# Performance work log

Hardware: AMD Instinct MI355X
Metric: run time of the kernel (lower is better)

## Reference

```python
import jax, jax.numpy as jnp
import numpy as np

NEMBED, EMBED_DIM, HID_DIM, OUT_DIM, NUM_CLASSES = 128, 64, 128, 128, 2
BATCH, TEAM = 2048, 5
N_OPS = 8


def setup_inputs() -> dict:
    key = jax.random.key(0)
    ks = jax.random.split(key, 8)
    w_eq = np.sqrt(2.0 / (EMBED_DIM + HID_DIM + N_OPS))
    return {
        "x": jax.random.randint(ks[0], (BATCH, 2, TEAM), 0, NEMBED, dtype=jnp.int32),
        "embed": jax.random.normal(ks[1], (NEMBED, EMBED_DIM), jnp.float32) * 0.1,
        "coefs1": jax.random.normal(ks[2], (EMBED_DIM, HID_DIM, N_OPS), jnp.float32) * w_eq,
        "bias1": jnp.zeros((HID_DIM,), jnp.float32),
        "wout1": jax.random.normal(ks[3], (HID_DIM, OUT_DIM), jnp.float32) * np.sqrt(1.0 / HID_DIM),
        "bout1": jnp.zeros((OUT_DIM,), jnp.float32),
        "coefs2": jax.random.normal(ks[4], (EMBED_DIM, HID_DIM, N_OPS), jnp.float32) * w_eq,
        "bias2": jnp.zeros((HID_DIM,), jnp.float32),
        "wout2": jax.random.normal(ks[5], (HID_DIM, OUT_DIM), jnp.float32) * np.sqrt(1.0 / HID_DIM),
        "bout2": jnp.zeros((OUT_DIM,), jnp.float32),
        "fcw": jax.random.normal(ks[6], (2 * OUT_DIM, NCLS := NUM_CLASSES and 2 * OUT_DIM and NUM_CLASSES), jnp.float32) * np.sqrt(1.0 / (2 * OUT_DIM)),
        "fcb": jnp.zeros((NUM_CLASSES,), jnp.float32),
    }


def eset_ops_3_to_3(t):
    # t: (N, D, m, m, m). 8 equivariant basis ops: keep-or-(sum&broadcast) each axis.
    # Pooled ops are kept with singleton dims; broadcasting happens after the
    # channel contraction (cheaper, same math as expand-then-contract).
    s1 = t.sum(-3, keepdims=True)
    s2 = t.sum(-2, keepdims=True)
    s3 = t.sum(-1, keepdims=True)
    s12 = t.sum((-3, -2), keepdims=True)
    s13 = t.sum((-3, -1), keepdims=True)
    s23 = t.sum((-2, -1), keepdims=True)
    sall = t.sum((-3, -2, -1), keepdims=True)
    return [t, s1, s2, s3, s12, s13, s23, sall]


def eq3_layer(t, coefs, bias):
    # coefs: (D_in, D_out, 8); output (N, D_out, m, m, m)
    ops = eset_ops_3_to_3(t)
    out = 0.0
    for b, op in enumerate(ops):
        out = out + jnp.einsum('ndijk,ds->nsijk', op, coefs[:, :, b])
    return out + bias[None, :, None, None, None]


def setnet3to3(t, coefs, bias, wout, bout):
    h = jax.nn.relu(eq3_layer(t, coefs, bias))          # (N, H, m, m, m)
    return jnp.einsum('nsijk,so->nijko', h, wout) + bout  # (N, m, m, m, out_dim)


def reference(x, embed, coefs1, bias1, wout1, bout1, coefs2, bias2, wout2, bout2, fcw, fcb):
    e1 = jax.nn.relu(embed[x[:, 0]])  # (N, 5, D)
    e2 = jax.nn.relu(embed[x[:, 1]])
    t1 = jnp.einsum('bid,bjd,bkd->bdijk', e1, e1, e1)  # (N, D, 5, 5, 5)
    t2 = jnp.einsum('bid,bjd,bkd->bdijk', e2, e2, e2)
    o1 = setnet3to3(t1, coefs1, bias1, wout1, bout1)
    o2 = setnet3to3(t2, coefs2, bias2, wout2, bout2)
    t1e = jax.nn.relu(o1.mean(axis=(1, 2, 3)))  # (N, out_dim)
    t2e = jax.nn.relu(o2.mean(axis=(1, 2, 3)))
    z = jnp.concatenate([t1e, t2e], axis=-1)    # dropout_prob=0 / eval mode: no-op
    return z @ fcw + fcb
```

## Files before the change

kernel.cpp:

```cpp
#include <hip/hip_runtime.h>


typedef __attribute__((ext_vector_type(8))) short bf16x8;
typedef __attribute__((ext_vector_type(4))) float f32x4;

#define DEV __device__ __forceinline__

DEV constexpr int pid2(int a, int b) {
  int x = a < b ? a : b;
  int y = a < b ? b : a;
  return x * (9 - x) / 2 + y;
}
DEV constexpr int tid3(int i, int j, int k) {
  int a = i, b = j, c = k, t;
  if (a > b) { t = a; a = b; b = t; }
  if (b > c) { t = b; b = c; c = t; }
  if (a > b) { t = a; a = b; b = t; }
  return a * (a * a - 18 * a + 107) / 6 + (b - a) * (11 - a - b) / 2 + (c - b);
}

DEV ushort f2bf(float f) {
  unsigned u = __builtin_bit_cast(unsigned, f);
  return (ushort)((u + 0x7FFFu + ((u >> 16) & 1u)) >> 16);
}

__global__ __launch_bounds__(256)
void cvt_prep_kernel(const float* __restrict__ c1, const float* __restrict__ c2,
                     const float* __restrict__ w1, const float* __restrict__ w2,
                     ushort* __restrict__ ct, float* __restrict__ wt, int do_wt) {
  const int idx = blockIdx.x * 256 + threadIdx.x;
  if (idx < 2 * 8 * 128 * 64) {
    const int d    = idx & 63;
    const int s    = (idx >> 6) & 127;
    const int b    = (idx >> 13) & 7;
    const int side = idx >> 16;
    const float* src = side ? c2 : c1;
    ct[idx] = f2bf(src[(d * 128 + s) * 8 + b]);
  } else if (do_wt) {
    const int j = idx - 131072;
    if (j < 2 * 128 * 128) {
      const int ss   = j & 127;
      const int o    = (j >> 7) & 127;
      const int side = j >> 14;
      wt[j] = (side ? w2 : w1)[ss * 128 + o];
    }
  }
}


__global__ __launch_bounds__(256, 4)
void dota2_eq3_side(const int* __restrict__ x, const float* __restrict__ embed,
                    const float* __restrict__ bias1, const float* __restrict__ bias2,
                    const float* __restrict__ wout1, const float* __restrict__ wout2,
                    const float* __restrict__ bout1, const float* __restrict__ bout2,
                    const float* __restrict__ fcw,
                    const ushort* __restrict__ ct, const float* __restrict__ wt,
                    float* __restrict__ pbuf)
{
  __shared__ __align__(16) ushort FT[80][72];
  __shared__ __align__(16) float  OUT[64][101];
  __shared__ __align__(16) float  scratch[256];
  __shared__ __align__(16) float  hbar[128];
  __shared__ __align__(16) float  zL[128];

  const int u    = blockIdx.x;
  const int side = u & 1;
  const int tid  = threadIdx.x;
  const int w    = tid >> 6;
  const int l    = tid & 63;
  const int grp  = l >> 4;
  const int lc   = l & 15;

  if (tid < 64) {
    const int d = tid;
    const int* xn = x + u * 5;
    float v[5];
    #pragma unroll
    for (int i = 0; i < 5; ++i) v[i] = fmaxf(embed[xn[i] * 64 + d], 0.f);
    const float S  = v[0] + v[1] + v[2] + v[3] + v[4];
    const float S2 = S * S;
    const float S3 = S2 * S;
    float p2[15];
    {
      int c2 = 0;
      #pragma unroll
      for (int a = 0; a < 5; ++a)
        #pragma unroll
        for (int b = a; b < 5; ++b) { p2[c2] = v[a] * v[b]; ++c2; }
    }
    ushort* colp = &FT[0][d];
    {
      int c3 = 0;
      #pragma unroll
      for (int a = 0; a < 5; ++a)
        #pragma unroll
        for (int b = a; b < 5; ++b)
          #pragma unroll
          for (int c = b; c < 5; ++c) { colp[c3 * 72] = f2bf(p2[pid2(a, b)] * v[c]); ++c3; }
    }
    #pragma unroll
    for (int t = 0; t < 15; ++t) colp[(48 + t) * 72] = f2bf(S * p2[t]);
    #pragma unroll
    for (int i = 0; i < 5; ++i)  colp[(64 + i) * 72] = f2bf(S2 * v[i]);
    colp[69 * 72] = f2bf(S3);
  } else {
    const int idx = tid - 64;
    #pragma unroll
    for (int e0 = 0; e0 < 9; ++e0) {
      const int e = idx + e0 * 192;
      const int r = e / 72;
      const int c = e - r * 72;
      const int row = (r < 13) ? (35 + r) : ((r == 13) ? 63 : (56 + r));
      FT[row][c] = 0;
    }
  }
  __syncthreads();

  const ushort* CTs = ct + side * (8 * 128 * 64);

  auto bfrag = [&](int t0, int kh) -> bf16x8 {
    return *(const bf16x8*)(&FT[t0 + lc][32 * kh + 8 * grp]);
  };
  auto dwrite = [&](const f32x4& acc, int s_local, int colbase, int nvalid) {
    if (lc < nvalid) {
      float* p = &OUT[s_local + 4 * grp][colbase + lc];
      p[0] = acc[0]; p[101] = acc[1]; p[202] = acc[2]; p[303] = acc[3];
    }
  };

  auto do_gemms = [&](int sh) {
    const int sg = 64 * sh + 16 * w;
    const int s_local = 16 * w;
    auto afrag = [&](int b, int kh) -> bf16x8 {
      const ushort* rp = CTs + (b * 128 + sg + lc) * 64;
      return *(const bf16x8*)(rp + 32 * kh + 8 * grp);
    };
    {
      const bf16x8 A0 = afrag(0, 0), A1 = afrag(0, 1);
      #pragma unroll
      for (int nt = 0; nt < 3; ++nt) {
        const bf16x8 B0 = bfrag(nt * 16, 0), B1 = bfrag(nt * 16, 1);
        f32x4 acc = {0.f, 0.f, 0.f, 0.f};
        acc = __builtin_amdgcn_mfma_f32_16x16x32_bf16(A0, B0, acc, 0, 0, 0);
        acc = __builtin_amdgcn_mfma_f32_16x16x32_bf16(A1, B1, acc, 0, 0, 0);
        dwrite(acc, s_local, nt * 16, (nt == 2) ? 3 : 16);
      }
    }
    {
      const bf16x8 B0 = bfrag(48, 0), B1 = bfrag(48, 1);
      #pragma unroll
      for (int b = 1; b <= 3; ++b) {
        const bf16x8 A0 = afrag(b, 0), A1 = afrag(b, 1);
        f32x4 acc = {0.f, 0.f, 0.f, 0.f};
        acc = __builtin_amdgcn_mfma_f32_16x16x32_bf16(A0, B0, acc, 0, 0, 0);
        acc = __builtin_amdgcn_mfma_f32_16x16x32_bf16(A1, B1, acc, 0, 0, 0);
        dwrite(acc, s_local, 35 + (b - 1) * 15, 15);
      }
    }
    {
      const bf16x8 B0 = bfrag(64, 0), B1 = bfrag(64, 1);
      #pragma unroll
      for (int b = 4; b <= 6; ++b) {
        const bf16x8 A0 = afrag(b, 0), A1 = afrag(b, 1);
        f32x4 acc = {0.f, 0.f, 0.f, 0.f};
        acc = __builtin_amdgcn_mfma_f32_16x16x32_bf16(A0, B0, acc, 0, 0, 0);
        acc = __builtin_amdgcn_mfma_f32_16x16x32_bf16(A1, B1, acc, 0, 0, 0);
        dwrite(acc, s_local, 80 + (b - 4) * 5, 5);
      }
      const bf16x8 A0 = afrag(7, 0), A1 = afrag(7, 1);
      f32x4 acc = {0.f, 0.f, 0.f, 0.f};
      acc = __builtin_amdgcn_mfma_f32_16x16x32_bf16(A0, B0, acc, 0, 0, 0);
      acc = __builtin_amdgcn_mfma_f32_16x16x32_bf16(A1, B1, acc, 0, 0, 0);
      if (lc == 5) {
        float* p = &OUT[s_local + 4 * grp][95];
        p[0] = acc[0]; p[101] = acc[1]; p[202] = acc[2]; p[303] = acc[3];
      }
    }
  };

  auto do_asm = [&](int sh) {
    const int ch = tid & 63;
    const int q  = tid >> 6;
    float T[96];
    #pragma unroll
    for (int t = 0; t < 96; ++t) T[t] = OUT[ch][t];
    const float* bi = side ? bias2 : bias1;
    const float base = T[95] + bi[64 * sh + ch];
    float hsum = 0.f;
    auto cell = [&](int c) {
      const int i = c / 25, j = (c / 5) % 5, k = c % 5;
      const float val = base + T[90 + i] + T[85 + j] + T[65 + pid2(i, j)]
                      + T[80 + k] + T[50 + pid2(i, k)] + T[35 + pid2(j, k)]
                      + T[tid3(i, j, k)];
      hsum += fmaxf(val, 0.f);
    };
    if (q == 0) {
      #pragma unroll
      for (int c = 0; c < 31; ++c) cell(c);
    } else if (q == 1) {
      #pragma unroll
      for (int c = 31; c < 62; ++c) cell(c);
    } else if (q == 2) {
      #pragma unroll
      for (int c = 62; c < 93; ++c) cell(c);
    } else {
      #pragma unroll
      for (int c = 93; c < 125; ++c) cell(c);
    }
    scratch[q * 64 + ch] = hsum;
  };

  do_gemms(0);
  __syncthreads();
  do_asm(0);
  __syncthreads();
  if (tid < 64)
    hbar[tid] = (scratch[tid] + scratch[64 + tid] + scratch[128 + tid] + scratch[192 + tid])
                * (1.f / 125.f);
  do_gemms(1);
  __syncthreads();
  do_asm(1);
  __syncthreads();
  if (tid < 64)
    hbar[64 + tid] = (scratch[tid] + scratch[64 + tid] + scratch[128 + tid] + scratch[192 + tid])
                     * (1.f / 125.f);
  __syncthreads();

  {
    const int o = tid & 127, shh = tid >> 7;
    float r;
    if (wt != nullptr) {
      const f32x4* wv = (const f32x4*)(wt + side * 16384 + o * 128 + shh * 64);
      const f32x4* hv = (const f32x4*)(&hbar[shh * 64]);
      float a0 = 0.f, a1 = 0.f, a2 = 0.f, a3 = 0.f;
      #pragma unroll
      for (int qq = 0; qq < 16; ++qq) {
        const f32x4 wq = wv[qq];
        const f32x4 hq = hv[qq];
        a0 = fmaf(hq[0], wq[0], a0);
        a1 = fmaf(hq[1], wq[1], a1);
        a2 = fmaf(hq[2], wq[2], a2);
        a3 = fmaf(hq[3], wq[3], a3);
      }
      r = (a0 + a1) + (a2 + a3);
    } else {
      const float* W = side ? wout2 : wout1;
      float a0 = 0.f, a1 = 0.f;
      #pragma unroll 8
      for (int ss = 64 * shh; ss < 64 * shh + 64; ss += 2) {
        a0 = fmaf(hbar[ss], W[ss * 128 + o], a0);
        a1 = fmaf(hbar[ss + 1], W[(ss + 1) * 128 + o], a1);
      }
      r = a0 + a1;
    }
    scratch[shh * 128 + o] = r;
  }
  __syncthreads();
  if (tid < 128) {
    const float* bo_ = side ? bout2 : bout1;
    zL[tid] = fmaxf(scratch[tid] + scratch[128 + tid] + bo_[tid], 0.f);
  }
  __syncthreads();

  if (tid < 64) {
    const float z0 = zL[tid], z1 = zL[tid + 64];
    const float* fw = fcw + side * 256;
    float p0 = fmaf(z0, fw[2 * tid],     z1 * fw[2 * tid + 128]);
    float p1 = fmaf(z0, fw[2 * tid + 1], z1 * fw[2 * tid + 129]);
    #pragma unroll
    for (int off = 32; off; off >>= 1) {
      p0 += __shfl_down(p0, off);
      p1 += __shfl_down(p1, off);
    }
    if (tid == 0) {
      pbuf[2 * u + 0] = p0;
      pbuf[2 * u + 1] = p1;
    }
  }
}

__global__ __launch_bounds__(256)
void fc_final(const float* __restrict__ pbuf, const float* __restrict__ fcb,
              float* __restrict__ out, int nout) {
  const int t = blockIdx.x * 256 + threadIdx.x;
  if (t < nout) {
    const int n = t >> 1, c = t & 1;
    out[t] = pbuf[4 * n + c] + pbuf[4 * n + 2 + c] + fcb[c];
  }
}

extern "C" void kernel_launch(void* const* d_in, const int* in_sizes, int n_in,
                              void* d_out, int out_size, void* d_ws, size_t ws_size,
                              hipStream_t stream) {
  const int*   x      = (const int*)  d_in[0];
  const float* embed  = (const float*)d_in[1];
  const float* coefs1 = (const float*)d_in[2];
  const float* bias1  = (const float*)d_in[3];
  const float* wout1  = (const float*)d_in[4];
  const float* bout1  = (const float*)d_in[5];
  const float* coefs2 = (const float*)d_in[6];
  const float* bias2  = (const float*)d_in[7];
  const float* wout2  = (const float*)d_in[8];
  const float* bout2  = (const float*)d_in[9];
  const float* fcw    = (const float*)d_in[10];
  const float* fcb    = (const float*)d_in[11];
  float* out = (float*)d_out;

  float*  pbuf = (float*)d_ws;
  ushort* ct   = (ushort*)((char*)d_ws + 32768);
  const int do_wt = (ws_size >= (size_t)(32768 + 262144 + 131072)) ? 1 : 0;
  float*  wt   = do_wt ? (float*)((char*)d_ws + 32768 + 262144) : nullptr;

  const int batch  = in_sizes[0] / 10;
  const int nunits = batch * 2;

  cvt_prep_kernel<<<640, 256, 0, stream>>>(coefs1, coefs2, wout1, wout2, ct, wt, do_wt);
  dota2_eq3_side<<<nunits, 256, 0, stream>>>(
      x, embed, bias1, bias2, wout1, wout2, bout1, bout2, fcw, ct, wt, pbuf);
  fc_final<<<(nunits + 255) / 256, 256, 0, stream>>>(pbuf, fcb, out, nunits);
}
```

Before: 103.5 us.

## Move cell assembly onto MFMA with 0/1 selection matrices and batch 8 units per block

The scalar per-cell assembly of the pooled terms is replaced by an MFMA contraction. A constant 0/1 selection matrix is built in registers, and the intermediate T is stored as bf16 in swizzled LDS, so relu and the mean are computed from MFMA accumulators. Each block now processes 8 units in a loop and overlaps the previous unit's FC epilogue with the next unit's feature build. This is meant to remove VALU-heavy assembly and per-block launch overhead, at the cost of fewer blocks (lower occupancy bound) and extra bf16 rounding of intermediates.

```diff
diff --git a/kernel.cpp b/kernel.cpp
--- a/kernel.cpp
+++ b/kernel.cpp
@@ -5,23 +5,33 @@
 typedef __attribute__((ext_vector_type(4))) float f32x4;
 
 #define DEV __device__ __forceinline__
-
-DEV constexpr int pid2(int a, int b) {
-  int x = a < b ? a : b;
-  int y = a < b ? b : a;
+#define MFMA __builtin_amdgcn_mfma_f32_16x16x32_bf16
+
+DEV constexpr int pid2c(int a, int b) {
+  int x = a < b ? a : b, y = a < b ? b : a;
   return x * (9 - x) / 2 + y;
 }
-DEV constexpr int tid3(int i, int j, int k) {
+DEV constexpr int tid3c(int i, int j, int k) {
   int a = i, b = j, c = k, t;
   if (a > b) { t = a; a = b; b = t; }
   if (b > c) { t = b; b = c; c = t; }
   if (a > b) { t = a; a = b; b = t; }
   return a * (a * a - 18 * a + 107) / 6 + (b - a) * (11 - a - b) / 2 + (c - b);
 }
-
+DEV int pid2r(int x, int y) { if (x > y) { int t = x; x = y; y = t; } return x * (9 - x) / 2 + y; }
+DEV int tid3r(int a, int b, int c) {
+  int t;
+  if (a > b) { t = a; a = b; b = t; }
+  if (b > c) { t = b; b = c; c = t; }
+  if (a > b) { t = a; a = b; b = t; }
+  return a * (a * a - 18 * a + 107) / 6 + (b - a) * (11 - a - b) / 2 + (c - b);
+}
 DEV ushort f2bf(float f) {
   unsigned u = __builtin_bit_cast(unsigned, f);
   return (ushort)((u + 0x7FFFu + ((u >> 16) & 1u)) >> 16);
+}
+DEV int t_addr(int s, int t) {
+  return s * 128 + ((((t >> 3) ^ (s & 7)) << 3) | (t & 7));
 }
 
 __global__ __launch_bounds__(256)
@@ -30,251 +40,314 @@
                      ushort* __restrict__ ct, float* __restrict__ wt, int do_wt) {
   const int idx = blockIdx.x * 256 + threadIdx.x;
   if (idx < 2 * 8 * 128 * 64) {
-    const int d    = idx & 63;
-    const int s    = (idx >> 6) & 127;
-    const int b    = (idx >> 13) & 7;
-    const int side = idx >> 16;
-    const float* src = side ? c2 : c1;
-    ct[idx] = f2bf(src[(d * 128 + s) * 8 + b]);
+    const int d = idx & 63, s = (idx >> 6) & 127, b = (idx >> 13) & 7, side = idx >> 16;
+    ct[idx] = f2bf((side ? c2 : c1)[(d * 128 + s) * 8 + b]);
   } else if (do_wt) {
     const int j = idx - 131072;
     if (j < 2 * 128 * 128) {
-      const int ss   = j & 127;
-      const int o    = (j >> 7) & 127;
-      const int side = j >> 14;
+      const int ss = j & 127, o = (j >> 7) & 127, side = j >> 14;
       wt[j] = (side ? w2 : w1)[ss * 128 + o];
     }
   }
 }
 
-
-__global__ __launch_bounds__(256, 4)
-void dota2_eq3_side(const int* __restrict__ x, const float* __restrict__ embed,
-                    const float* __restrict__ bias1, const float* __restrict__ bias2,
-                    const float* __restrict__ wout1, const float* __restrict__ wout2,
-                    const float* __restrict__ bout1, const float* __restrict__ bout2,
-                    const float* __restrict__ fcw,
-                    const ushort* __restrict__ ct, const float* __restrict__ wt,
-                    float* __restrict__ pbuf)
+__global__ __launch_bounds__(256, 2)
+void dota2_eq3_fused(const int* __restrict__ x, const float* __restrict__ embed,
+                     const float* __restrict__ bias1, const float* __restrict__ bias2,
+                     const float* __restrict__ bout1, const float* __restrict__ bout2,
+                     const float* __restrict__ wout1, const float* __restrict__ wout2,
+                     const float* __restrict__ fcw,
+                     const ushort* __restrict__ ct, const float* __restrict__ wt,
+                     float* __restrict__ pbuf, int nunits)
 {
   __shared__ __align__(16) ushort FT[80][72];
-  __shared__ __align__(16) float  OUT[64][101];
-  __shared__ __align__(16) float  scratch[256];
+  __shared__ __align__(16) ushort Tlds[128 * 128];
   __shared__ __align__(16) float  hbar[128];
-  __shared__ __align__(16) float  zL[128];
-
-  const int u    = blockIdx.x;
-  const int side = u & 1;
-  const int tid  = threadIdx.x;
-  const int w    = tid >> 6;
-  const int l    = tid & 63;
-  const int grp  = l >> 4;
-  const int lc   = l & 15;
-
-  if (tid < 64) {
-    const int d = tid;
-    const int* xn = x + u * 5;
-    float v[5];
+  __shared__ __align__(16) float  scratch[2][128];
+  __shared__ __align__(16) float  fcp[4];
+
+  const int tid = threadIdx.x;
+  const int w   = tid >> 6;
+  const int l   = tid & 63;
+  const int grp = l >> 4;
+  const int lc  = l & 15;
+
+  const int u0 = blockIdx.x * 8;
+  const int nu = (nunits - u0 < 8) ? (nunits - u0) : 8;
+  if (nu <= 0) return;
+
+  for (int e = tid; e < 1728; e += 256) {
+    const int r = e / 72, c = e - r * 72;
+    const int row = (r < 13) ? (35 + r) : ((r == 13) ? 63 : (70 + r - 14));
+    FT[row][c] = 0;
+  }
+  for (int e = tid; e < 2048; e += 256) {
+    const int s = e >> 4, t = 112 + (e & 15);
+    Tlds[t_addr(s, t)] = 0;
+  }
+
+  unsigned msk[8][4];
+  #pragma unroll
+  for (int mt = 0; mt < 8; ++mt) {
+    unsigned m0 = 0, m1 = 0, m2 = 0, m3 = 0;
+    const int cell = 16 * mt + lc;
+    if (cell <= 124) {
+      const int i = cell / 25, rm = cell - 25 * i, j = rm / 5, k = rm - 5 * j;
+      int tv[8];
+      tv[0] = tid3r(i, j, k);
+      tv[1] = 48 + pid2r(j, k);
+      tv[2] = 64 + pid2r(i, k);
+      tv[3] = 80 + pid2r(i, j);
+      tv[4] = 96 + k;
+      tv[5] = 101 + j;
+      tv[6] = 106 + i;
+      tv[7] = 111;
+      #pragma unroll
+      for (int e = 0; e < 8; ++e) {
+        const unsigned b = 1u << (tv[e] & 31);
+        const int dw = tv[e] >> 5;
+        m0 |= (dw == 0) ? b : 0u;
+        m1 |= (dw == 1) ? b : 0u;
+        m2 |= (dw == 2) ? b : 0u;
+        m3 |= (dw == 3) ? b : 0u;
+      }
+    }
+    msk[mt][0] = m0; msk[mt][1] = m1; msk[mt][2] = m2; msk[mt][3] = m3;
+  }
+  bf16x8 af[8][4];
+  #pragma unroll
+  for (int mt = 0; mt < 8; ++mt)
     #pragma unroll
-    for (int i = 0; i < 5; ++i) v[i] = fmaxf(embed[xn[i] * 64 + d], 0.f);
-    const float S  = v[0] + v[1] + v[2] + v[3] + v[4];
-    const float S2 = S * S;
-    const float S3 = S2 * S;
-    float p2[15];
+    for (int kt = 0; kt < 4; ++kt) {
+      const unsigned by = (msk[mt][kt] >> (8 * grp)) & 0xFFu;
+      unsigned fr[4];
+      #pragma unroll
+      for (int qd = 0; qd < 4; ++qd)
+        fr[qd] = (((by >> (2 * qd)) & 1u) * 0x3F80u) |
+                 (((by >> (2 * qd + 1)) & 1u) * 0x3F800000u);
+      af[mt][kt] = __builtin_bit_cast(bf16x8, *(const bf16x8*)fr);
+    }
+  __syncthreads();
+
+  auto ftfrag = [&](int row0, int kt) -> bf16x8 {
+    return *(const bf16x8*)(&FT[row0 + lc][8 * grp + 32 * kt]);
+  };
+  auto twrite64 = [&](int s, int t0, const f32x4& a) {
+    uint2 pk;
+    pk.x = (unsigned)f2bf(a[0]) | ((unsigned)f2bf(a[1]) << 16);
+    pk.y = (unsigned)f2bf(a[2]) | ((unsigned)f2bf(a[3]) << 16);
+    *(uint2*)(Tlds + t_addr(s, t0)) = pk;
+  };
+
+  for (int uu = 0; uu < nu; ++uu) {
+    const int u = u0 + uu;
+    const int side = u & 1;
+
     {
-      int c2 = 0;
+      const int d = tid & 63, q = tid >> 6;
+      const int* xn = x + u * 5;
+      float vv[5];
+      #pragma unroll
+      for (int i = 0; i < 5; ++i) vv[i] = fmaxf(embed[xn[i] * 64 + d], 0.f);
+      const float S = vv[0] + vv[1] + vv[2] + vv[3] + vv[4];
+      const float S2 = S * S, S3 = S2 * S;
+      float p2[15];
       #pragma unroll
       for (int a = 0; a < 5; ++a)
         #pragma unroll
-        for (int b = a; b < 5; ++b) { p2[c2] = v[a] * v[b]; ++c2; }
-    }
-    ushort* colp = &FT[0][d];
-    {
-      int c3 = 0;
+        for (int b = a; b < 5; ++b) p2[pid2c(a, b)] = vv[a] * vv[b];
       #pragma unroll
       for (int a = 0; a < 5; ++a)
         #pragma unroll
         for (int b = a; b < 5; ++b)
           #pragma unroll
-          for (int c = b; c < 5; ++c) { colp[c3 * 72] = f2bf(p2[pid2(a, b)] * v[c]); ++c3; }
-    }
-    #pragma unroll
-    for (int t = 0; t < 15; ++t) colp[(48 + t) * 72] = f2bf(S * p2[t]);
-    #pragma unroll
-    for (int i = 0; i < 5; ++i)  colp[(64 + i) * 72] = f2bf(S2 * v[i]);
-    colp[69 * 72] = f2bf(S3);
-  } else {
-    const int idx = tid - 64;
-    #pragma unroll
-    for (int e0 = 0; e0 < 9; ++e0) {
-      const int e = idx + e0 * 192;
-      const int r = e / 72;
-      const int c = e - r * 72;
-      const int row = (r < 13) ? (35 + r) : ((r == 13) ? 63 : (56 + r));
-      FT[row][c] = 0;
-    }
-  }
-  __syncthreads();
-
-  const ushort* CTs = ct + side * (8 * 128 * 64);
-
-  auto bfrag = [&](int t0, int kh) -> bf16x8 {
-    return *(const bf16x8*)(&FT[t0 + lc][32 * kh + 8 * grp]);
-  };
-  auto dwrite = [&](const f32x4& acc, int s_local, int colbase, int nvalid) {
-    if (lc < nvalid) {
-      float* p = &OUT[s_local + 4 * grp][colbase + lc];
-      p[0] = acc[0]; p[101] = acc[1]; p[202] = acc[2]; p[303] = acc[3];
-    }
-  };
-
-  auto do_gemms = [&](int sh) {
-    const int sg = 64 * sh + 16 * w;
-    const int s_local = 16 * w;
-    auto afrag = [&](int b, int kh) -> bf16x8 {
-      const ushort* rp = CTs + (b * 128 + sg + lc) * 64;
-      return *(const bf16x8*)(rp + 32 * kh + 8 * grp);
-    };
+          for (int c = b; c < 5; ++c) {
+            const int c3 = tid3c(a, b, c);
+            const int qq = (c3 < 14) ? 0 : (c3 < 28) ? 1 : 2;
+            if (q == qq) FT[c3][d] = f2bf(p2[pid2c(a, b)] * vv[c]);
+          }
+      #pragma unroll
+      for (int p = 0; p < 15; ++p) {
+        const int qq = (p < 8) ? 2 : 3;
+        if (q == qq) FT[48 + p][d] = f2bf(S * p2[p]);
+      }
+      if (q == 3) {
+        #pragma unroll
+        for (int i = 0; i < 5; ++i) FT[64 + i][d] = f2bf(S2 * vv[i]);
+        FT[69][d] = f2bf(S3);
+      }
+    }
+    if (uu > 0 && tid < 128) {
+      const int o = tid;
+      const int sp = (u - 1) & 1;
+      const float* bo = sp ? bout2 : bout1;
+      const float z = fmaxf(scratch[0][o] + scratch[1][o] + bo[o], 0.f);
+      const float* fw = fcw + sp * 256;
+      float p0 = z * fw[2 * o], p1 = z * fw[2 * o + 1];
+      #pragma unroll
+      for (int off = 32; off; off >>= 1) {
+        p0 += __shfl_down(p0, off);
+        p1 += __shfl_down(p1, off);
+      }
+      if ((tid & 63) == 0) { fcp[(tid >> 6) * 2] = p0; fcp[(tid >> 6) * 2 + 1] = p1; }
+    }
+    __syncthreads();
+
     {
-      const bf16x8 A0 = afrag(0, 0), A1 = afrag(0, 1);
-      #pragma unroll
-      for (int nt = 0; nt < 3; ++nt) {
-        const bf16x8 B0 = bfrag(nt * 16, 0), B1 = bfrag(nt * 16, 1);
-        f32x4 acc = {0.f, 0.f, 0.f, 0.f};
-        acc = __builtin_amdgcn_mfma_f32_16x16x32_bf16(A0, B0, acc, 0, 0, 0);
-        acc = __builtin_amdgcn_mfma_f32_16x16x32_bf16(A1, B1, acc, 0, 0, 0);
-        dwrite(acc, s_local, nt * 16, (nt == 2) ? 3 : 16);
-      }
-    }
+      if (tid == 0 && uu > 0) {
+        pbuf[2 * (u - 1)]     = fcp[0] + fcp[2];
+        pbuf[2 * (u - 1) + 1] = fcp[1] + fcp[3];
+      }
+      const ushort* CTs = ct + side * (8 * 128 * 64);
+      auto cfrag = [&](int bank, int ntI, int kt) -> bf16x8 {
+        const ushort* rp = CTs + (size_t)(bank * 128 + 32 * w + 16 * ntI + lc) * 64
+                         + 32 * kt + 8 * grp;
+        return *(const bf16x8*)rp;
+      };
+      const int sA = 32 * w + lc;
+      const int sB = sA + 16;
+
+      {
+        const bf16x8 B00 = cfrag(0, 0, 0), B01 = cfrag(0, 0, 1);
+        const bf16x8 B10 = cfrag(0, 1, 0), B11 = cfrag(0, 1, 1);
+        #pragma unroll
+        for (int mtl = 0; mtl < 3; ++mtl) {
+          const bf16x8 A0 = ftfrag(16 * mtl, 0), A1 = ftfrag(16 * mtl, 1);
+          f32x4 a = {0.f, 0.f, 0.f, 0.f};
+          a = MFMA(A0, B00, a, 0, 0, 0);
+          a = MFMA(A1, B01, a, 0, 0, 0);
+          twrite64(sA, 16 * mtl + 4 * grp, a);
+          f32x4 b = {0.f, 0.f, 0.f, 0.f};
+          b = MFMA(A0, B10, b, 0, 0, 0);
+          b = MFMA(A1, B11, b, 0, 0, 0);
+          twrite64(sB, 16 * mtl + 4 * grp, b);
+        }
+      }
+      {
+        const bf16x8 AP0 = ftfrag(48, 0), AP1 = ftfrag(48, 1);
+        #pragma unroll
+        for (int bank = 1; bank <= 3; ++bank) {
+          const int tb = 48 + 16 * (bank - 1);
+          const bf16x8 B0 = cfrag(bank, 0, 0), B1 = cfrag(bank, 0, 1);
+          f32x4 a = {0.f, 0.f, 0.f, 0.f};
+          a = MFMA(AP0, B0, a, 0, 0, 0);
+          a = MFMA(AP1, B1, a, 0, 0, 0);
+          twrite64(sA, tb + 4 * grp, a);
+          const bf16x8 C0 = cfrag(bank, 1, 0), C1 = cfrag(bank, 1, 1);
+          f32x4 b = {0.f, 0.f, 0.f, 0.f};
+          b = MFMA(AP0, C0, b, 0, 0, 0);
+          b = MFMA(AP1, C1, b, 0, 0, 0);
+          twrite64(sB, tb + 4 * grp, b);
+        }
+      }
+      {
+        const bf16x8 AS0 = ftfrag(64, 0), AS1 = ftfrag(64, 1);
+        #pragma unroll
+        for (int bank = 4; bank <= 7; ++bank) {
+          const int tb = (bank < 7) ? (96 + 5 * (bank - 4)) : 111;
+          #pragma unroll
+          for (int ntI = 0; ntI < 2; ++ntI) {
+            const int s = (ntI == 0) ? sA : sB;
+            const bf16x8 B0 = cfrag(bank, ntI, 0), B1 = cfrag(bank, ntI, 1);
+            f32x4 a = {0.f, 0.f, 0.f, 0.f};
+            a = MFMA(AS0, B0, a, 0, 0, 0);
+            a = MFMA(AS1, B1, a, 0, 0, 0);
+            if (bank < 7) {
+              if (grp == 0) {
+                #pragma unroll
+                for (int r = 0; r < 4; ++r) Tlds[t_addr(s, tb + r)] = f2bf(a[r]);
+              } else if (grp == 1) {
+                Tlds[t_addr(s, tb + 4)] = f2bf(a[0]);
+              }
+            } else {
+              if (grp == 1) Tlds[t_addr(s, 111)] = f2bf(a[1]);
+            }
+          }
+        }
+      }
+      const float* bi = side ? bias2 : bias1;
+      #pragma unroll
+      for (int ntI = 0; ntI < 2; ++ntI) {
+        const int s = (ntI == 0) ? sA : sB;
+        const float bsv = bi[s];
+        f32x4 acc[8];
+        #pragma unroll
+        for (int mt = 0; mt < 8; ++mt) acc[mt] = {bsv, bsv, bsv, bsv};
+        #pragma unroll
+        for (int kt = 0; kt < 4; ++kt) {
+          const bf16x8 Bf = *(const bf16x8*)(Tlds + t_addr(s, 32 * kt + 8 * grp));
+          #pragma unroll
+          for (int mt = 0; mt < 8; ++mt)
+            acc[mt] = MFMA(af[mt][kt], Bf, acc[mt], 0, 0, 0);
+        }
+        float hs = 0.f;
+        #pragma unroll
+        for (int mt = 0; mt < 8; ++mt)
+          #pragma unroll
+          for (int r = 0; r < 4; ++r) {
+            float v = fmaxf(acc[mt][r], 0.f);
+            if (mt == 7 && r >= 1) v = (grp == 3) ? 0.f : v;
+            hs += v;
+          }
+        hs += __shfl_xor(hs, 16);
+        hs += __shfl_xor(hs, 32);
+        if (grp == 0) hbar[s] = hs * (1.f / 125.f);
+      }
+    }
+    __syncthreads();
+
     {
-      const bf16x8 B0 = bfrag(48, 0), B1 = bfrag(48, 1);
-      #pragma unroll
-      for (int b = 1; b <= 3; ++b) {
-        const bf16x8 A0 = afrag(b, 0), A1 = afrag(b, 1);
-        f32x4 acc = {0.f, 0.f, 0.f, 0.f};
-        acc = __builtin_amdgcn_mfma_f32_16x16x32_bf16(A0, B0, acc, 0, 0, 0);
-        acc = __builtin_amdgcn_mfma_f32_16x16x32_bf16(A1, B1, acc, 0, 0, 0);
-        dwrite(acc, s_local, 35 + (b - 1) * 15, 15);
-      }
-    }
-    {
-      const bf16x8 B0 = bfrag(64, 0), B1 = bfrag(64, 1);
-      #pragma unroll
-      for (int b = 4; b <= 6; ++b) {
-        const bf16x8 A0 = afrag(b, 0), A1 = afrag(b, 1);
-        f32x4 acc = {0.f, 0.f, 0.f, 0.f};
-        acc = __builtin_amdgcn_mfma_f32_16x16x32_bf16(A0, B0, acc, 0, 0, 0);
-        acc = __builtin_amdgcn_mfma_f32_16x16x32_bf16(A1, B1, acc, 0, 0, 0);
-        dwrite(acc, s_local, 80 + (b - 4) * 5, 5);
-      }
-      const bf16x8 A0 = afrag(7, 0), A1 = afrag(7, 1);
-      f32x4 acc = {0.f, 0.f, 0.f, 0.f};
-      acc = __builtin_amdgcn_mfma_f32_16x16x32_bf16(A0, B0, acc, 0, 0, 0);
-      acc = __builtin_amdgcn_mfma_f32_16x16x32_bf16(A1, B1, acc, 0, 0, 0);
-      if (lc == 5) {
-        float* p = &OUT[s_local + 4 * grp][95];
-        p[0] = acc[0]; p[101] = acc[1]; p[202] = acc[2]; p[303] = acc[3];
-      }
-    }
-  };
-
-  auto do_asm = [&](int sh) {
-    const int ch = tid & 63;
-    const int q  = tid >> 6;
-    float T[96];
-    #pragma unroll
-    for (int t = 0; t < 96; ++t) T[t] = OUT[ch][t];
-    const float* bi = side ? bias2 : bias1;
-    const float base = T[95] + bi[64 * sh + ch];
-    float hsum = 0.f;
-    auto cell = [&](int c) {
-      const int i = c / 25, j = (c / 5) % 5, k = c % 5;
-      const float val = base + T[90 + i] + T[85 + j] + T[65 + pid2(i, j)]
-                      + T[80 + k] + T[50 + pid2(i, k)] + T[35 + pid2(j, k)]
-                      + T[tid3(i, j, k)];
-      hsum += fmaxf(val, 0.f);
-    };
-    if (q == 0) {
-      #pragma unroll
-      for (int c = 0; c < 31; ++c) cell(c);
-    } else if (q == 1) {
-      #pragma unroll
-      for (int c = 31; c < 62; ++c) cell(c);
-    } else if (q == 2) {
-      #pragma unroll
-      for (int c = 62; c < 93; ++c) cell(c);
-    } else {
-      #pragma unroll
-      for (int c = 93; c < 125; ++c) cell(c);
-    }
-    scratch[q * 64 + ch] = hsum;
-  };
-
-  do_gemms(0);
-  __syncthreads();
-  do_asm(0);
-  __syncthreads();
-  if (tid < 64)
-    hbar[tid] = (scratch[tid] + scratch[64 + tid] + scratch[128 + tid] + scratch[192 + tid])
-                * (1.f / 125.f);
-  do_gemms(1);
-  __syncthreads();
-  do_asm(1);
-  __syncthreads();
-  if (tid < 64)
-    hbar[64 + tid] = (scratch[tid] + scratch[64 + tid] + scratch[128 + tid] + scratch[192 + tid])
-                     * (1.f / 125.f);
-  __syncthreads();
+      const int o = tid & 127, shh = tid >> 7;
+      float r;
+      if (wt != nullptr) {
+        const f32x4* wv = (const f32x4*)(wt + side * 16384 + o * 128 + shh * 64);
+        const f32x4* hv = (const f32x4*)(&hbar[shh * 64]);
+        float a0 = 0.f, a1 = 0.f, a2 = 0.f, a3 = 0.f;
+        #pragma unroll
+        for (int qq = 0; qq < 16; ++qq) {
+          const f32x4 wq = wv[qq];
+          const f32x4 hq = hv[qq];
+          a0 = fmaf(hq[0], wq[0], a0);
+          a1 = fmaf(hq[1], wq[1], a1);
+          a2 = fmaf(hq[2], wq[2], a2);
+          a3 = fmaf(hq[3], wq[3], a3);
+        }
+        r = (a0 + a1) + (a2 + a3);
+      } else {
+        const float* W = side ? wout2 : wout1;
+        float a0 = 0.f, a1 = 0.f;
+        #pragma unroll 8
+        for (int ss = 64 * shh; ss < 64 * shh + 64; ss += 2) {
+          a0 = fmaf(hbar[ss], W[ss * 128 + o], a0);
+          a1 = fmaf(hbar[ss + 1], W[(ss + 1) * 128 + o], a1);
+        }
+        r = a0 + a1;
+      }
+      scratch[shh][o] = r;
+    }
+    __syncthreads();
+  }
 
   {
-    const int o = tid & 127, shh = tid >> 7;
-    float r;
-    if (wt != nullptr) {
-      const f32x4* wv = (const f32x4*)(wt + side * 16384 + o * 128 + shh * 64);
-      const f32x4* hv = (const f32x4*)(&hbar[shh * 64]);
-      float a0 = 0.f, a1 = 0.f, a2 = 0.f, a3 = 0.f;
-      #pragma unroll
-      for (int qq = 0; qq < 16; ++qq) {
-        const f32x4 wq = wv[qq];
-        const f32x4 hq = hv[qq];
-        a0 = fmaf(hq[0], wq[0], a0);
-        a1 = fmaf(hq[1], wq[1], a1);
-        a2 = fmaf(hq[2], wq[2], a2);
-        a3 = fmaf(hq[3], wq[3], a3);
-      }
-      r = (a0 + a1) + (a2 + a3);
-    } else {
-      const float* W = side ? wout2 : wout1;
-      float a0 = 0.f, a1 = 0.f;
-      #pragma unroll 8
-      for (int ss = 64 * shh; ss < 64 * shh + 64; ss += 2) {
-        a0 = fmaf(hbar[ss], W[ss * 128 + o], a0);
-        a1 = fmaf(hbar[ss + 1], W[(ss + 1) * 128 + o], a1);
-      }
-      r = a0 + a1;
-    }
-    scratch[shh * 128 + o] = r;
-  }
-  __syncthreads();
-  if (tid < 128) {
-    const float* bo_ = side ? bout2 : bout1;
-    zL[tid] = fmaxf(scratch[tid] + scratch[128 + tid] + bo_[tid], 0.f);
-  }
-  __syncthreads();
-
-  if (tid < 64) {
-    const float z0 = zL[tid], z1 = zL[tid + 64];
-    const float* fw = fcw + side * 256;
-    float p0 = fmaf(z0, fw[2 * tid],     z1 * fw[2 * tid + 128]);
-    float p1 = fmaf(z0, fw[2 * tid + 1], z1 * fw[2 * tid + 129]);
-    #pragma unroll
-    for (int off = 32; off; off >>= 1) {
-      p0 += __shfl_down(p0, off);
-      p1 += __shfl_down(p1, off);
-    }
+    const int ul = u0 + nu - 1;
+    if (tid < 128) {
+      const int o = tid;
+      const int sp = ul & 1;
+      const float* bo = sp ? bout2 : bout1;
+      const float z = fmaxf(scratch[0][o] + scratch[1][o] + bo[o], 0.f);
+      const float* fw = fcw + sp * 256;
+      float p0 = z * fw[2 * o], p1 = z * fw[2 * o + 1];
+      #pragma unroll
+      for (int off = 32; off; off >>= 1) {
+        p0 += __shfl_down(p0, off);
+        p1 += __shfl_down(p1, off);
+      }
+      if ((tid & 63) == 0) { fcp[(tid >> 6) * 2] = p0; fcp[(tid >> 6) * 2 + 1] = p1; }
+    }
+    __syncthreads();
     if (tid == 0) {
-      pbuf[2 * u + 0] = p0;
-      pbuf[2 * u + 1] = p1;
+      pbuf[2 * ul]     = fcp[0] + fcp[2];
+      pbuf[2 * ul + 1] = fcp[1] + fcp[3];
     }
   }
 }
@@ -313,9 +386,10 @@
 
   const int batch  = in_sizes[0] / 10;
   const int nunits = batch * 2;
+  const int nblk   = (nunits + 7) / 8;
 
   cvt_prep_kernel<<<640, 256, 0, stream>>>(coefs1, coefs2, wout1, wout2, ct, wt, do_wt);
-  dota2_eq3_side<<<nunits, 256, 0, stream>>>(
-      x, embed, bias1, bias2, wout1, wout2, bout1, bout2, fcw, ct, wt, pbuf);
+  dota2_eq3_fused<<<nblk, 256, 0, stream>>>(
+      x, embed, bias1, bias2, bout1, bout2, wout1, wout2, fcw, ct, wt, pbuf, nunits);
   fc_final<<<(nunits + 255) / 256, 256, 0, stream>>>(pbuf, fcb, out, nunits);
 }
```

Result: slower. 137.0 us (+32.3%).
